# Performance work log

Hardware: AMD Instinct MI355X
Metric: run time of the kernel (lower is better)

Reference implementation:

```python
import jax, jax.numpy as jnp
import numpy as np

EPS = 0.1          # perturbation scale (init kwarg eps)
NORM_EPS = 1e-12   # torch F.normalize clamp


def spmm(row, col, val, x, n):
    # sparse COO matmul: out[row] += val * x[col]
    return jax.ops.segment_sum(val[:, None] * x[col], row, num_segments=n)


def setup_inputs() -> dict:
    key = jax.random.key(0)
    ks = jax.random.split(key, 6)
    U, I, D, NNZ, L = 100000, 50000, 64, 2000000, 3
    N = U + I
    return {
        "user_emb": jax.random.normal(ks[0], (U, D), dtype=jnp.float32),
        "item_emb": jax.random.normal(ks[1], (I, D), dtype=jnp.float32),
        "adj_row": jax.random.randint(ks[2], (NNZ,), 0, N, dtype=jnp.int64),
        "adj_col": jax.random.randint(ks[3], (NNZ,), 0, N, dtype=jnp.int64),
        "adj_val": jax.random.uniform(ks[4], (NNZ,), dtype=jnp.float32),
        "noise": jax.random.uniform(ks[5], (L, N, D), dtype=jnp.float32),
    }


def reference(user_emb, item_emb, adj_row, adj_col, adj_val, noise):
    U = user_emb.shape[0]
    N = U + item_emb.shape[0]
    L = noise.shape[0]
    ego = jnp.concatenate([user_emb, item_emb], axis=0)  # [N, D]
    layer_sum = jnp.zeros_like(ego)
    for k in range(L):
        ego = spmm(adj_row, adj_col, adj_val, ego, N)
        # perturbed branch: ego += sign(ego) * L2-normalize(noise_k) * eps
        rn = noise[k]
        rn = rn / jnp.maximum(jnp.linalg.norm(rn, axis=-1, keepdims=True), NORM_EPS)
        ego = ego + jnp.sign(ego) * rn * EPS
        layer_sum = layer_sum + ego
    all_emb = layer_sum / L  # mean over stacked layers
    return all_emb[:U], all_emb[U:]
```

## Files before the change

kernel.cpp:

```cpp
#include <hip/hip_runtime.h>
#include <hip/hip_fp16.h>

#define DDIM 64
#define EPS 0.1f
#define NORM_EPS 1e-12f

__global__ void init_zero_kernel(const float* __restrict__ user, const float* __restrict__ item,
                                 float* __restrict__ egoA, float* __restrict__ egoB,
                                 int UD, int ND) {
    int i = blockIdx.x * blockDim.x + threadIdx.x;
    if (i < ND) {
        egoA[i] = (i < UD) ? user[i] : item[i - UD];
        egoB[i] = 0.0f;
    }
}

__global__ void zero_int_kernel(int* __restrict__ p, int n) {
    int i = blockIdx.x * blockDim.x + threadIdx.x;
    if (i < n) p[i] = 0;
}

__global__ void hist_kernel(const int* __restrict__ row, int* __restrict__ cnt,
                            int* __restrict__ pos, int nnz) {
    int e = blockIdx.x * blockDim.x + threadIdx.x;
    if (e < nnz) pos[e] = atomicAdd(&cnt[row[e]], 1);
}

__global__ void scan1_kernel(const int* __restrict__ cnt, int* __restrict__ partial,
                             int* __restrict__ bsums, int n) {
    __shared__ int s[1024];
    int i = blockIdx.x * 1024 + threadIdx.x;
    int v = (i < n) ? cnt[i] : 0;
    s[threadIdx.x] = v;
    __syncthreads();
    for (int off = 1; off < 1024; off <<= 1) {
        int t = (threadIdx.x >= off) ? s[threadIdx.x - off] : 0;
        __syncthreads();
        s[threadIdx.x] += t;
        __syncthreads();
    }
    if (i < n) partial[i] = s[threadIdx.x];
    if (threadIdx.x == 1023) bsums[blockIdx.x] = s[1023];
}

__global__ void scan2_kernel(int* __restrict__ bsums, int nb) {
    if (blockIdx.x == 0 && threadIdx.x == 0) {
        int run = 0;
        for (int b = 0; b < nb; ++b) { int t = bsums[b]; bsums[b] = run; run += t; }
    }
}

__global__ void scan3_serialbs_kernel(const int* __restrict__ partial, const int* __restrict__ bsums,
                                      int* __restrict__ rowptr, int n) {
    int i = blockIdx.x * 1024 + threadIdx.x;
    if (i < n) rowptr[i + 1] = partial[i] + bsums[blockIdx.x];
    if (i == 0) rowptr[0] = 0;
}

__global__ void scan3_fused_kernel(const int* __restrict__ partial, const int* __restrict__ bsums,
                                   int* __restrict__ rowptr, int n, int nb) {
    __shared__ int s[1024];
    int t = threadIdx.x;
    s[t] = (t < nb && t < (int)blockIdx.x) ? bsums[t] : 0;
    __syncthreads();
    #pragma unroll
    for (int off = 512; off > 0; off >>= 1) {
        if (t < off) s[t] += s[t + off];
        __syncthreads();
    }
    int base = s[0];
    int i = blockIdx.x * 1024 + t;
    if (i < n) rowptr[i + 1] = partial[i] + base;
    if (i == 0) rowptr[0] = 0;
}

__global__ void scatter_kernel(const int* __restrict__ row, const int* __restrict__ col,
                               const float* __restrict__ val, const int* __restrict__ rowptr,
                               const int* __restrict__ pos, int2* __restrict__ edges, int nnz) {
    int e = blockIdx.x * blockDim.x + threadIdx.x;
    if (e < nnz) {
        int r = row[e];
        edges[rowptr[r] + pos[e]] = make_int2(col[e], __float_as_int(val[e]));
    }
}

__device__ __forceinline__ void acc_half8(float f[8], const uint4& q, float v) {
    __half2 h; float2 t;
    h = *reinterpret_cast<const __half2*>(&q.x); t = __half22float2(h);
    f[0] = fmaf(v, t.x, f[0]); f[1] = fmaf(v, t.y, f[1]);
    h = *reinterpret_cast<const __half2*>(&q.y); t = __half22float2(h);
    f[2] = fmaf(v, t.x, f[2]); f[3] = fmaf(v, t.y, f[3]);
    h = *reinterpret_cast<const __half2*>(&q.z); t = __half22float2(h);
    f[4] = fmaf(v, t.x, f[4]); f[5] = fmaf(v, t.y, f[5]);
    h = *reinterpret_cast<const __half2*>(&q.w); t = __half22float2(h);
    f[6] = fmaf(v, t.x, f[6]); f[7] = fmaf(v, t.y, f[7]);
}

template <int XHALF>
__global__ void fused_layer_kernel(const int* __restrict__ rowptr, const int2* __restrict__ edges,
                                   const float4* __restrict__ xu4, const float4* __restrict__ xi4,
                                   int splitRow,
                                   const uint4* __restrict__ x16,
                                   const float4* __restrict__ noise4,
                                   uint4* __restrict__ y16, float4* __restrict__ out4,
                                   int N, int first, float invL) {
    int lane = threadIdx.x & 63;
    int r = (blockIdx.x * blockDim.x + threadIdx.x) >> 6;
    if (r >= N) return;
    int g   = lane >> 3;
    int sub = lane & 7;

    float4 nva = make_float4(0.f,0.f,0.f,0.f), nvb = make_float4(0.f,0.f,0.f,0.f);
    float4 poa = make_float4(0.f,0.f,0.f,0.f), pob = make_float4(0.f,0.f,0.f,0.f);
    size_t f4idx = (size_t)r * 16 + sub * 2;
    if (g == 0) {
        nva = noise4[f4idx]; nvb = noise4[f4idx + 1];
        if (!first) { poa = out4[f4idx]; pob = out4[f4idx + 1]; }
    }

    int beg = __builtin_amdgcn_readfirstlane(rowptr[r]);
    int end = __builtin_amdgcn_readfirstlane(rowptr[r + 1]);

    float f[8] = {0.f,0.f,0.f,0.f,0.f,0.f,0.f,0.f};

    for (int e = beg; e < end; e += 16) {
        int last = end - 1;
        int e0 = e + g, e1 = e + 8 + g;
        int2 ed0 = edges[min(e0, last)];
        int2 ed1 = edges[min(e1, last)];
        float v0 = (e0 < end) ? __int_as_float(ed0.y) : 0.0f;
        float v1 = (e1 < end) ? __int_as_float(ed1.y) : 0.0f;
        if (XHALF) {
            uint4 q0 = x16[(size_t)ed0.x * 8 + sub];
            uint4 q1 = x16[(size_t)ed1.x * 8 + sub];
            acc_half8(f, q0, v0);
            acc_half8(f, q1, v1);
        } else {
            const float4* s0 = (ed0.x < splitRow) ? (xu4 + (size_t)ed0.x * 16)
                                                  : (xi4 + (size_t)(ed0.x - splitRow) * 16);
            const float4* s1 = (ed1.x < splitRow) ? (xu4 + (size_t)ed1.x * 16)
                                                  : (xi4 + (size_t)(ed1.x - splitRow) * 16);
            float4 a0 = s0[sub * 2], b0 = s0[sub * 2 + 1];
            float4 a1 = s1[sub * 2], b1 = s1[sub * 2 + 1];
            f[0]=fmaf(v0,a0.x,f[0]); f[1]=fmaf(v0,a0.y,f[1]); f[2]=fmaf(v0,a0.z,f[2]); f[3]=fmaf(v0,a0.w,f[3]);
            f[4]=fmaf(v0,b0.x,f[4]); f[5]=fmaf(v0,b0.y,f[5]); f[6]=fmaf(v0,b0.z,f[6]); f[7]=fmaf(v0,b0.w,f[7]);
            f[0]=fmaf(v1,a1.x,f[0]); f[1]=fmaf(v1,a1.y,f[1]); f[2]=fmaf(v1,a1.z,f[2]); f[3]=fmaf(v1,a1.w,f[3]);
            f[4]=fmaf(v1,b1.x,f[4]); f[5]=fmaf(v1,b1.y,f[5]); f[6]=fmaf(v1,b1.z,f[6]); f[7]=fmaf(v1,b1.w,f[7]);
        }
    }

    #pragma unroll
    for (int off = 8; off <= 32; off <<= 1) {
        #pragma unroll
        for (int i = 0; i < 8; ++i) f[i] += __shfl_xor(f[i], off, 64);
    }

    if (g == 0) {
        float sq = nva.x*nva.x + nva.y*nva.y + nva.z*nva.z + nva.w*nva.w
                 + nvb.x*nvb.x + nvb.y*nvb.y + nvb.z*nvb.z + nvb.w*nvb.w;
        #pragma unroll
        for (int off = 1; off <= 4; off <<= 1) sq += __shfl_xor(sq, off, 64);
        float scale = EPS / fmaxf(sqrtf(sq), NORM_EPS);

        float nse[8] = {nva.x,nva.y,nva.z,nva.w,nvb.x,nvb.y,nvb.z,nvb.w};
        float po[8]  = {poa.x,poa.y,poa.z,poa.w,pob.x,pob.y,pob.z,pob.w};
        float ep[8];
        #pragma unroll
        for (int i = 0; i < 8; ++i) {
            float s = (f[i] > 0.f) ? 1.f : ((f[i] < 0.f) ? -1.f : 0.f);
            ep[i] = f[i] + s * nse[i] * scale;
        }
        if (y16) {
            __half2 h0 = __floats2half2_rn(ep[0], ep[1]);
            __half2 h1 = __floats2half2_rn(ep[2], ep[3]);
            __half2 h2 = __floats2half2_rn(ep[4], ep[5]);
            __half2 h3 = __floats2half2_rn(ep[6], ep[7]);
            uint4 st;
            st.x = *reinterpret_cast<unsigned*>(&h0);
            st.y = *reinterpret_cast<unsigned*>(&h1);
            st.z = *reinterpret_cast<unsigned*>(&h2);
            st.w = *reinterpret_cast<unsigned*>(&h3);
            y16[(size_t)r * 8 + sub] = st;
        }
        float4 oa, ob;
        if (first) {
            oa = make_float4(ep[0]*invL, ep[1]*invL, ep[2]*invL, ep[3]*invL);
            ob = make_float4(ep[4]*invL, ep[5]*invL, ep[6]*invL, ep[7]*invL);
        } else {
            oa = make_float4(fmaf(ep[0],invL,po[0]), fmaf(ep[1],invL,po[1]),
                             fmaf(ep[2],invL,po[2]), fmaf(ep[3],invL,po[3]));
            ob = make_float4(fmaf(ep[4],invL,po[4]), fmaf(ep[5],invL,po[5]),
                             fmaf(ep[6],invL,po[6]), fmaf(ep[7],invL,po[7]));
        }
        out4[f4idx] = oa;
        out4[f4idx + 1] = ob;
    }
}

__global__ void spmm_kernel(const int* __restrict__ row, const int* __restrict__ col,
                            const float* __restrict__ val, const float* __restrict__ x,
                            float* __restrict__ y, int nnz) {
    int gtid = blockIdx.x * blockDim.x + threadIdx.x;
    int wid = gtid >> 6;
    int lane = threadIdx.x & 63;
    int nwaves = (gridDim.x * blockDim.x) >> 6;
    for (int e = wid; e < nnz; e += nwaves) {
        int r = row[e];
        int c = col[e];
        float v = val[e];
        unsafeAtomicAdd(&y[(size_t)r * DDIM + lane], v * x[(size_t)c * DDIM + lane]);
    }
}

__global__ void perturb_kernel(float* __restrict__ ego, const float* __restrict__ noise,
                               float* __restrict__ zero_buf, float* __restrict__ out,
                               int N, int first, float invL) {
    int gtid = blockIdx.x * blockDim.x + threadIdx.x;
    int wid = gtid >> 6;
    int lane = threadIdx.x & 63;
    int nwaves = (gridDim.x * blockDim.x) >> 6;
    for (int n = wid; n < N; n += nwaves) {
        size_t idx = (size_t)n * DDIM + lane;
        float nv = noise[idx];
        float sq = nv * nv;
        #pragma unroll
        for (int off = 32; off > 0; off >>= 1) sq += __shfl_xor(sq, off, 64);
        float rn = nv / fmaxf(sqrtf(sq), NORM_EPS);
        float e = ego[idx];
        float s = (e > 0.0f) ? 1.0f : ((e < 0.0f) ? -1.0f : 0.0f);
        float ep = e + s * rn * EPS;
        ego[idx] = ep;
        if (zero_buf) zero_buf[idx] = 0.0f;
        float o = ep * invL;
        out[idx] = first ? o : (out[idx] + o);
    }
}

extern "C" void kernel_launch(void* const* d_in, const int* in_sizes, int n_in,
                              void* d_out, int out_size, void* d_ws, size_t ws_size,
                              hipStream_t stream) {
    const float* user  = (const float*)d_in[0];
    const float* item  = (const float*)d_in[1];
    const int*   row   = (const int*)d_in[2];
    const int*   col   = (const int*)d_in[3];
    const float* val   = (const float*)d_in[4];
    const float* noise = (const float*)d_in[5];
    float* out = (float*)d_out;

    int UD = in_sizes[0];
    int ID = in_sizes[1];
    int ND = UD + ID;
    int N  = ND / DDIM;
    int nnz = in_sizes[2];
    int L  = in_sizes[5] / ND;
    float invL = 1.0f / (float)L;

    size_t ND_ = (size_t)ND;
    size_t ofs_rowptr  = ND_;
    size_t ofs_cnt     = ofs_rowptr + (size_t)(N + 2);
    size_t ofs_partial = ofs_cnt + (size_t)N;
    size_t ofs_bsums   = ofs_partial + (size_t)N;
    size_t ofs_pos     = ofs_bsums + 1024;
    size_t ofs_edges   = ofs_pos + (size_t)nnz;
    size_t needed = (ofs_edges + 2ull * (size_t)nnz) * 4ull;

    if (ws_size >= needed && (N % 2) == 0 && (nnz % 2) == 0 && (UD % DDIM) == 0) {
        uint4* ego16A = (uint4*)d_ws;
        uint4* ego16B = (uint4*)((char*)d_ws + 2ull * ND_);
        int* rowptr  = (int*)d_ws + ofs_rowptr;
        int* cnt     = (int*)d_ws + ofs_cnt;
        int* partial = (int*)d_ws + ofs_partial;
        int* bsums   = (int*)d_ws + ofs_bsums;
        int* pos     = (int*)d_ws + ofs_pos;
        int2* edges  = (int2*)((int*)d_ws + ofs_edges);

        int nb = (N + 1023) / 1024;

        zero_int_kernel<<<(N + 255) / 256, 256, 0, stream>>>(cnt, N);
        hist_kernel<<<(nnz + 255) / 256, 256, 0, stream>>>(row, cnt, pos, nnz);
        scan1_kernel<<<nb, 1024, 0, stream>>>(cnt, partial, bsums, N);
        if (nb <= 1024) {
            scan3_fused_kernel<<<nb, 1024, 0, stream>>>(partial, bsums, rowptr, N, nb);
        } else {
            scan2_kernel<<<1, 64, 0, stream>>>(bsums, nb);
            scan3_serialbs_kernel<<<nb, 1024, 0, stream>>>(partial, bsums, rowptr, N);
        }
        scatter_kernel<<<(nnz + 255) / 256, 256, 0, stream>>>(row, col, val, rowptr, pos, edges, nnz);

        const float4* user4 = (const float4*)user;
        const float4* item4 = (const float4*)item;
        const float4* noise4 = (const float4*)noise;
        float4* out4 = (float4*)out;
        int Urows = UD / DDIM;

        int blocks = (N * 64 + 255) / 256;
        uint4* e16[2] = { ego16A, ego16B };
        for (int k = 0; k < L; ++k) {
            uint4* y = (k == L - 1) ? nullptr : e16[k & 1];
            const float4* nz = noise4 + (size_t)k * (ND_ / 4);
            if (k == 0) {
                fused_layer_kernel<0><<<blocks, 256, 0, stream>>>(
                    rowptr, edges, user4, item4, Urows, nullptr,
                    nz, y, out4, N, 1, invL);
            } else {
                fused_layer_kernel<1><<<blocks, 256, 0, stream>>>(
                    rowptr, edges, nullptr, nullptr, 0, (const uint4*)e16[(k - 1) & 1],
                    nz, y, out4, N, 0, invL);
            }
        }
    } else {
        float* egoA = (float*)d_ws;
        float* egoB = egoA + ND_;
        init_zero_kernel<<<(ND + 255) / 256, 256, 0, stream>>>(user, item, egoA, egoB, UD, ND);
        float* cur = egoA;
        float* nxt = egoB;
        for (int k = 0; k < L; ++k) {
            spmm_kernel<<<2048, 256, 0, stream>>>(row, col, val, cur, nxt, nnz);
            perturb_kernel<<<1024, 256, 0, stream>>>(
                nxt, noise + (size_t)k * ND_,
                (k + 1 < L) ? cur : nullptr, out, N, (k == 0) ? 1 : 0, invL);
            float* t = cur; cur = nxt; nxt = t;
        }
    }
}
```

Before: 375.9 us.

## Map one row per 8-lane group and use fma_mix for half accumulation

Each layer kernel now assigns one row per 8-lane group, so a wavefront processes 8 rows instead of one, instead of splitting a row's edges across the whole wavefront. This removes the cross-group shuffle reductions and the padded, clamped edge loads. The half-precision gather now uses inline v_fma_mix_f32 to fuse the convert and FMA. The cost is that lanes within a wavefront diverge when neighboring rows have different degrees, and each row's edges are walked serially by its group.

Result: faster. 356.6 us (-5.2%).

```diff
diff --git a/kernel.cpp b/kernel.cpp
--- a/kernel.cpp
+++ b/kernel.cpp
@@ -84,16 +84,20 @@
     }
 }
 
-__device__ __forceinline__ void acc_half8(float f[8], const uint4& q, float v) {
-    __half2 h; float2 t;
-    h = *reinterpret_cast<const __half2*>(&q.x); t = __half22float2(h);
-    f[0] = fmaf(v, t.x, f[0]); f[1] = fmaf(v, t.y, f[1]);
-    h = *reinterpret_cast<const __half2*>(&q.y); t = __half22float2(h);
-    f[2] = fmaf(v, t.x, f[2]); f[3] = fmaf(v, t.y, f[3]);
-    h = *reinterpret_cast<const __half2*>(&q.z); t = __half22float2(h);
-    f[4] = fmaf(v, t.x, f[4]); f[5] = fmaf(v, t.y, f[5]);
-    h = *reinterpret_cast<const __half2*>(&q.w); t = __half22float2(h);
-    f[6] = fmaf(v, t.x, f[6]); f[7] = fmaf(v, t.y, f[7]);
+__device__ __forceinline__ void fma_mix8(float& f0, float& f1, float& f2, float& f3,
+                                         float& f4, float& f5, float& f6, float& f7,
+                                         uint4 q, float v) {
+    asm("v_fma_mix_f32 %0, %8, %12, %0 op_sel:[0,0,0] op_sel_hi:[1,0,0]\n\t"
+        "v_fma_mix_f32 %1, %8, %12, %1 op_sel:[1,0,0] op_sel_hi:[1,0,0]\n\t"
+        "v_fma_mix_f32 %2, %9, %12, %2 op_sel:[0,0,0] op_sel_hi:[1,0,0]\n\t"
+        "v_fma_mix_f32 %3, %9, %12, %3 op_sel:[1,0,0] op_sel_hi:[1,0,0]\n\t"
+        "v_fma_mix_f32 %4, %10, %12, %4 op_sel:[0,0,0] op_sel_hi:[1,0,0]\n\t"
+        "v_fma_mix_f32 %5, %10, %12, %5 op_sel:[1,0,0] op_sel_hi:[1,0,0]\n\t"
+        "v_fma_mix_f32 %6, %11, %12, %6 op_sel:[0,0,0] op_sel_hi:[1,0,0]\n\t"
+        "v_fma_mix_f32 %7, %11, %12, %7 op_sel:[1,0,0] op_sel_hi:[1,0,0]"
+        : "+v"(f0), "+v"(f1), "+v"(f2), "+v"(f3),
+          "+v"(f4), "+v"(f5), "+v"(f6), "+v"(f7)
+        : "v"(q.x), "v"(q.y), "v"(q.z), "v"(q.w), "v"(v));
 }
 
 template <int XHALF>
@@ -105,71 +109,74 @@
                                    uint4* __restrict__ y16, float4* __restrict__ out4,
                                    int N, int first, float invL) {
     int lane = threadIdx.x & 63;
-    int r = (blockIdx.x * blockDim.x + threadIdx.x) >> 6;
-    if (r >= N) return;
+    int wid = (blockIdx.x * blockDim.x + threadIdx.x) >> 6;
     int g   = lane >> 3;
     int sub = lane & 7;
+    int r = wid * 8 + g;
+    bool active = r < N;
+
+    size_t f4idx = (size_t)r * 16 + sub * 2;
 
     float4 nva = make_float4(0.f,0.f,0.f,0.f), nvb = make_float4(0.f,0.f,0.f,0.f);
     float4 poa = make_float4(0.f,0.f,0.f,0.f), pob = make_float4(0.f,0.f,0.f,0.f);
-    size_t f4idx = (size_t)r * 16 + sub * 2;
-    if (g == 0) {
+    int beg = 0, end = 0;
+    if (active) {
+        beg = rowptr[r];
+        end = rowptr[r + 1];
         nva = noise4[f4idx]; nvb = noise4[f4idx + 1];
         if (!first) { poa = out4[f4idx]; pob = out4[f4idx + 1]; }
     }
 
-    int beg = __builtin_amdgcn_readfirstlane(rowptr[r]);
-    int end = __builtin_amdgcn_readfirstlane(rowptr[r + 1]);
-
-    float f[8] = {0.f,0.f,0.f,0.f,0.f,0.f,0.f,0.f};
-
-    for (int e = beg; e < end; e += 16) {
-        int last = end - 1;
-        int e0 = e + g, e1 = e + 8 + g;
-        int2 ed0 = edges[min(e0, last)];
-        int2 ed1 = edges[min(e1, last)];
-        float v0 = (e0 < end) ? __int_as_float(ed0.y) : 0.0f;
-        float v1 = (e1 < end) ? __int_as_float(ed1.y) : 0.0f;
-        if (XHALF) {
+    float f0=0.f,f1=0.f,f2=0.f,f3=0.f,f4=0.f,f5=0.f,f6=0.f,f7=0.f;
+
+    int e = beg;
+    if (XHALF) {
+        while (e + 2 <= end) {
+            int2 ed0 = edges[e];
+            int2 ed1 = edges[e + 1];
             uint4 q0 = x16[(size_t)ed0.x * 8 + sub];
             uint4 q1 = x16[(size_t)ed1.x * 8 + sub];
-            acc_half8(f, q0, v0);
-            acc_half8(f, q1, v1);
-        } else {
-            const float4* s0 = (ed0.x < splitRow) ? (xu4 + (size_t)ed0.x * 16)
-                                                  : (xi4 + (size_t)(ed0.x - splitRow) * 16);
-            const float4* s1 = (ed1.x < splitRow) ? (xu4 + (size_t)ed1.x * 16)
-                                                  : (xi4 + (size_t)(ed1.x - splitRow) * 16);
-            float4 a0 = s0[sub * 2], b0 = s0[sub * 2 + 1];
-            float4 a1 = s1[sub * 2], b1 = s1[sub * 2 + 1];
-            f[0]=fmaf(v0,a0.x,f[0]); f[1]=fmaf(v0,a0.y,f[1]); f[2]=fmaf(v0,a0.z,f[2]); f[3]=fmaf(v0,a0.w,f[3]);
-            f[4]=fmaf(v0,b0.x,f[4]); f[5]=fmaf(v0,b0.y,f[5]); f[6]=fmaf(v0,b0.z,f[6]); f[7]=fmaf(v0,b0.w,f[7]);
-            f[0]=fmaf(v1,a1.x,f[0]); f[1]=fmaf(v1,a1.y,f[1]); f[2]=fmaf(v1,a1.z,f[2]); f[3]=fmaf(v1,a1.w,f[3]);
-            f[4]=fmaf(v1,b1.x,f[4]); f[5]=fmaf(v1,b1.y,f[5]); f[6]=fmaf(v1,b1.z,f[6]); f[7]=fmaf(v1,b1.w,f[7]);
-        }
-    }
-
+            fma_mix8(f0,f1,f2,f3,f4,f5,f6,f7, q0, __int_as_float(ed0.y));
+            fma_mix8(f0,f1,f2,f3,f4,f5,f6,f7, q1, __int_as_float(ed1.y));
+            e += 2;
+        }
+        if (e < end) {
+            int2 ed = edges[e];
+            uint4 q = x16[(size_t)ed.x * 8 + sub];
+            fma_mix8(f0,f1,f2,f3,f4,f5,f6,f7, q, __int_as_float(ed.y));
+        }
+    } else {
+        while (e < end) {
+            int2 ed = edges[e];
+            float v = __int_as_float(ed.y);
+            const float4* s = (ed.x < splitRow) ? (xu4 + (size_t)ed.x * 16)
+                                                : (xi4 + (size_t)(ed.x - splitRow) * 16);
+            float4 a = s[sub * 2], b = s[sub * 2 + 1];
+            f0 = fmaf(v, a.x, f0); f1 = fmaf(v, a.y, f1);
+            f2 = fmaf(v, a.z, f2); f3 = fmaf(v, a.w, f3);
+            f4 = fmaf(v, b.x, f4); f5 = fmaf(v, b.y, f5);
+            f6 = fmaf(v, b.z, f6); f7 = fmaf(v, b.w, f7);
+            ++e;
+        }
+    }
+
+    float sq = nva.x*nva.x + nva.y*nva.y + nva.z*nva.z + nva.w*nva.w
+             + nvb.x*nvb.x + nvb.y*nvb.y + nvb.z*nvb.z + nvb.w*nvb.w;
     #pragma unroll
-    for (int off = 8; off <= 32; off <<= 1) {
-        #pragma unroll
-        for (int i = 0; i < 8; ++i) f[i] += __shfl_xor(f[i], off, 64);
-    }
-
-    if (g == 0) {
-        float sq = nva.x*nva.x + nva.y*nva.y + nva.z*nva.z + nva.w*nva.w
-                 + nvb.x*nvb.x + nvb.y*nvb.y + nvb.z*nvb.z + nvb.w*nvb.w;
-        #pragma unroll
-        for (int off = 1; off <= 4; off <<= 1) sq += __shfl_xor(sq, off, 64);
-        float scale = EPS / fmaxf(sqrtf(sq), NORM_EPS);
-
-        float nse[8] = {nva.x,nva.y,nva.z,nva.w,nvb.x,nvb.y,nvb.z,nvb.w};
-        float po[8]  = {poa.x,poa.y,poa.z,poa.w,pob.x,pob.y,pob.z,pob.w};
-        float ep[8];
-        #pragma unroll
-        for (int i = 0; i < 8; ++i) {
-            float s = (f[i] > 0.f) ? 1.f : ((f[i] < 0.f) ? -1.f : 0.f);
-            ep[i] = f[i] + s * nse[i] * scale;
-        }
+    for (int off = 1; off <= 4; off <<= 1) sq += __shfl_xor(sq, off, 64);
+    float scale = EPS / fmaxf(sqrtf(sq), NORM_EPS);
+
+    float acc[8] = {f0,f1,f2,f3,f4,f5,f6,f7};
+    float nse[8] = {nva.x,nva.y,nva.z,nva.w,nvb.x,nvb.y,nvb.z,nvb.w};
+    float po[8]  = {poa.x,poa.y,poa.z,poa.w,pob.x,pob.y,pob.z,pob.w};
+    float ep[8];
+    #pragma unroll
+    for (int i = 0; i < 8; ++i) {
+        float s = (acc[i] > 0.f) ? 1.f : ((acc[i] < 0.f) ? -1.f : 0.f);
+        ep[i] = acc[i] + s * nse[i] * scale;
+    }
+
+    if (active) {
         if (y16) {
             __half2 h0 = __floats2half2_rn(ep[0], ep[1]);
             __half2 h1 = __floats2half2_rn(ep[2], ep[3]);
@@ -293,7 +300,7 @@
         float4* out4 = (float4*)out;
         int Urows = UD / DDIM;
 
-        int blocks = (N * 64 + 255) / 256;
+        int blocks = ((N * 8) + 255) / 256;
         uint4* e16[2] = { ego16A, ego16B };
         for (int k = 0; k < L; ++k) {
             uint4* y = (k == L - 1) ? nullptr : e16[k & 1];
```
